# Optimization experiments

Measured on AMD Instinct MI355X. Metric: run time of the kernel, lower is better.

The kernel has to match this reference:

```python
import jax, jax.numpy as jnp
import numpy as np

HEADS = 4
DIM_HEAD = 32
GROUPS = 32  # min(256//4, 32)
EPS = 1e-5


def setup_inputs() -> dict:
    key = jax.random.key(0)
    ks = jax.random.split(key, 5)
    B, C, H, W = 16, 256, 64, 64
    CD, HC, WC = 512, 32, 32
    hid = HEADS * DIM_HEAD  # 128
    return {
        "x": jax.random.normal(ks[0], (B, C, H, W), jnp.float32),
        "cond": jax.random.normal(ks[1], (B, CD, HC, WC), jnp.float32),
        "gn_w": jnp.ones((C,), jnp.float32),
        "gn_b": jnp.zeros((C,), jnp.float32),
        "w_q": jax.random.normal(ks[2], (hid, C), jnp.float32) * 0.05,
        "b_q": jnp.zeros((hid,), jnp.float32),
        "w_kv": jax.random.normal(ks[3], (2 * hid, CD), jnp.float32) * 0.05,
        "b_kv": jnp.zeros((2 * hid,), jnp.float32),
        "w_out": jax.random.normal(ks[4], (C, hid), jnp.float32) * 0.05,
        "b_out": jnp.zeros((C,), jnp.float32),
    }


def _group_norm(x, w, b):
    # x: (B, C, H, W); normalize per group over (channels-in-group, H, W)
    B, C, H, W = x.shape
    xg = x.reshape(B, GROUPS, C // GROUPS, H, W)
    mu = jnp.mean(xg, axis=(2, 3, 4), keepdims=True)
    var = jnp.var(xg, axis=(2, 3, 4), keepdims=True)
    xn = ((xg - mu) * jax.lax.rsqrt(var + EPS)).reshape(B, C, H, W)
    return xn * w[None, :, None, None] + b[None, :, None, None]


def _conv1x1(x, w, b):
    # x: (B, Cin, H, W), w: (Cout, Cin), b: (Cout,)
    return jnp.einsum('oc,bchw->bohw', w, x) + b[None, :, None, None]


def reference(x, cond, gn_w, gn_b, w_q, b_q, w_kv, b_kv, w_out, b_out):
    B, C, H, W = x.shape
    hid = HEADS * DIM_HEAD
    xn = _group_norm(x, gn_w, gn_b)
    q = _conv1x1(xn, w_q, b_q)          # (B, hid, H, W)
    kv = _conv1x1(cond, w_kv, b_kv)     # (B, 2*hid, Hc, Wc)
    Nc = kv.shape[2] * kv.shape[3]
    N = H * W
    k = kv[:, :hid].reshape(B, HEADS, DIM_HEAD, Nc)
    v = kv[:, hid:].reshape(B, HEADS, DIM_HEAD, Nc)
    q = q.reshape(B, HEADS, DIM_HEAD, N)
    k = jax.nn.softmax(k, axis=-1)
    # kv outer product: (B, heads, d, e)
    context = jnp.einsum('bhdn,bhen->bhde', k, v)
    # query contraction over d: (B, heads, e, n)
    out = jnp.einsum('bhde,bhdn->bhen', context, q)
    out = out.reshape(B, hid, H, W)
    return _conv1x1(out, w_out, b_out)
```

## Files before the change

kernel.cpp:

```cpp
#include <hip/hip_runtime.h>
#include <hip/hip_bf16.h>

typedef __attribute__((ext_vector_type(8))) short bf16x8;
typedef __attribute__((ext_vector_type(4))) float f32x4;

__device__ __forceinline__ ushort f2bf(float f) {
    __hip_bfloat16 h = __float2bfloat16(f);
    return __builtin_bit_cast(ushort, h);
}
__device__ __forceinline__ float bflo(unsigned u) { return __uint_as_float(u << 16); }
__device__ __forceinline__ float bfhi(unsigned u) { return __uint_as_float(u & 0xffff0000u); }

__device__ __forceinline__ void unpack8(uint4 r, float* o) {
    o[0] = bflo(r.x); o[1] = bfhi(r.x); o[2] = bflo(r.y); o[3] = bfhi(r.y);
    o[4] = bflo(r.z); o[5] = bfhi(r.z); o[6] = bflo(r.w); o[7] = bfhi(r.w);
}

__device__ __forceinline__ void gload16(const void* g, void* l) {
    __builtin_amdgcn_global_load_lds(
        (const __attribute__((address_space(1))) unsigned*)g,
        (__attribute__((address_space(3))) unsigned*)l,
        16, 0, 0);
}

__global__ void cvtw_kernel(const float* __restrict__ w, ushort* __restrict__ o,
                            float* __restrict__ zbase) {
    int i = blockIdx.x * 256 + threadIdx.x;
    if (i < 68608) zbase[i] = 0.f;
    o[i] = f2bf(w[i]);
}

__global__ __launch_bounds__(256) void kvstats_kernel(const ushort* __restrict__ wkv16,
                                                      const float* __restrict__ cond,
                                                      const float* __restrict__ b_kv,
                                                      ushort* __restrict__ kv16,
                                                      const float* __restrict__ x,
                                                      float* __restrict__ statacc) {
    __shared__ ushort lA[64 * 64];
    __shared__ ushort lB[64 * 64];
    __shared__ float scratch[64 * 64];
    __shared__ float ls[4], lss[4];
    int bid = blockIdx.x;
    int t = threadIdx.x;
    if (bid < 1024) {
        int nb = bid & 15, ob = (bid >> 4) & 3, b = bid >> 6;
        int col0 = nb * 64, row0 = ob * 64;
        int l = t & 63, wid = t >> 6;
        int wr = wid >> 1, wc = wid & 1;
        int lr = l & 15, lg = l >> 4;
        const ushort* Ab = wkv16 + (size_t)row0 * 512;
        const float* Bb = cond + (size_t)b * 512 * 1024 + col0;
        int sp = t & 31, sj = t >> 5;
        f32x4 acc[2][2] = {};
        for (int k0 = 0; k0 < 512; k0 += 64) {
            #pragma unroll
            for (int j = 0; j < 2; ++j) {
                int gi = j * 256 + t;
                int r = gi >> 3, g = (gi & 7) ^ (r & 7);
                gload16(Ab + (size_t)r * 512 + k0 + g * 8, (char*)lA + gi * 16);
            }
            #pragma unroll
            for (int j = 0; j < 4; ++j) {
                int s = j * 256 + t;
                int r = s >> 4, g = s & 15;
                float4 v = *(const float4*)&Bb[(size_t)(k0 + r) * 1024 + g * 4];
                int gs = g ^ ((r >> 1) & 15);
                *(float4*)((char*)scratch + r * 256 + gs * 16) = v;
            }
            __syncthreads();
            {
                int swz = sp & 15;
                float4 a0 = *(const float4*)((char*)scratch + (2*sp) * 256 + ((2*sj) ^ swz) * 16);
                float4 a1 = *(const float4*)((char*)scratch + (2*sp) * 256 + ((2*sj+1) ^ swz) * 16);
                float4 b0 = *(const float4*)((char*)scratch + (2*sp+1) * 256 + ((2*sj) ^ swz) * 16);
                float4 b1 = *(const float4*)((char*)scratch + (2*sp+1) * 256 + ((2*sj+1) ^ swz) * 16);
                float c0v[8] = {a0.x, a0.y, a0.z, a0.w, a1.x, a1.y, a1.z, a1.w};
                float c1v[8] = {b0.x, b0.y, b0.z, b0.w, b1.x, b1.y, b1.z, b1.w};
                #pragma unroll
                for (int w = 0; w < 8; ++w) {
                    int n = sj * 8 + w;
                    unsigned pk = (unsigned)f2bf(c0v[w]) | ((unsigned)f2bf(c1v[w]) << 16);
                    *(unsigned*)((char*)lB + n * 128 + (((sp >> 2) ^ (n & 7)) * 16) + (sp & 3) * 4) = pk;
                }
            }
            __syncthreads();
            #pragma unroll
            for (int ks = 0; ks < 2; ++ks) {
                bf16x8 av[2], bv[2];
                #pragma unroll
                for (int mi = 0; mi < 2; ++mi) {
                    int ar = wr * 32 + mi * 16 + lr;
                    int q = (ks * 4 + lg) ^ (ar & 7);
                    av[mi] = *(const bf16x8*)((const char*)lA + ar * 128 + q * 16);
                }
                #pragma unroll
                for (int ni = 0; ni < 2; ++ni) {
                    int br = wc * 32 + ni * 16 + lr;
                    int q = (ks * 4 + lg) ^ (br & 7);
                    bv[ni] = *(const bf16x8*)((const char*)lB + br * 128 + q * 16);
                }
                #pragma unroll
                for (int mi = 0; mi < 2; ++mi)
                    #pragma unroll
                    for (int ni = 0; ni < 2; ++ni)
                        acc[mi][ni] = __builtin_amdgcn_mfma_f32_16x16x32_bf16(
                            av[mi], bv[ni], acc[mi][ni], 0, 0, 0);
            }
            __syncthreads();
        }
        int orow = row0 + wr * 32, ocol = col0 + wc * 32 + lr;
        #pragma unroll
        for (int mi = 0; mi < 2; ++mi) {
            int rb = orow + mi * 16 + lg * 4;
            float4 b4 = *(const float4*)&b_kv[rb];
            float bvr[4] = {b4.x, b4.y, b4.z, b4.w};
            #pragma unroll
            for (int ni = 0; ni < 2; ++ni) {
                int cc = ocol + ni * 16;
                #pragma unroll
                for (int r = 0; r < 4; ++r)
                    kv16[((size_t)b * 256 + rb + r) * 1024 + cc] = f2bf(acc[mi][ni][r] + bvr[r]);
            }
        }
    } else {
        int bg = bid - 1024;
        const float4* xp = (const float4*)(x + (size_t)bg * 32768);
        float s = 0.f, ss = 0.f;
        for (int i = t; i < 8192; i += 256) {
            float4 v = xp[i];
            s  += v.x + v.y + v.z + v.w;
            ss += v.x*v.x + v.y*v.y + v.z*v.z + v.w*v.w;
        }
        #pragma unroll
        for (int off = 32; off > 0; off >>= 1) {
            s  += __shfl_down(s, off, 64);
            ss += __shfl_down(ss, off, 64);
        }
        int wave = t >> 6;
        if ((t & 63) == 0) { ls[wave] = s; lss[wave] = ss; }
        __syncthreads();
        if (t == 0) {
            statacc[bg * 2]     = ls[0] + ls[1] + ls[2] + ls[3];
            statacc[bg * 2 + 1] = lss[0] + lss[1] + lss[2] + lss[3];
        }
    }
}

__global__ __launch_bounds__(256) void ctx_partial_kernel(const ushort* __restrict__ kv,
                                                          float* __restrict__ rowsum,
                                                          float* __restrict__ ctx) {
    int bh = blockIdx.y, b = bh >> 2, h = bh & 3;
    int n0 = blockIdx.x * 128;
    __shared__ float pl[32][129], vl[32][129];
    int t = threadIdx.x;
    int r = t >> 3, cs = (t & 7) * 16;
    const ushort* kp = kv + ((size_t)b * 256 + h * 32 + r) * 1024 + n0 + cs;
    const ushort* vp = kv + ((size_t)b * 256 + 128 + h * 32 + r) * 1024 + n0 + cs;
    float kvals[16], vvals[16];
    unpack8(((const uint4*)kp)[0], kvals);
    unpack8(((const uint4*)kp)[1], kvals + 8);
    unpack8(((const uint4*)vp)[0], vvals);
    unpack8(((const uint4*)vp)[1], vvals + 8);
    float psum = 0.f;
    #pragma unroll
    for (int i = 0; i < 16; ++i) {
        float e = __expf(kvals[i]);
        pl[r][cs + i] = e;
        vl[r][cs + i] = vvals[i];
        psum += e;
    }
    psum += __shfl_xor(psum, 1, 64);
    psum += __shfl_xor(psum, 2, 64);
    psum += __shfl_xor(psum, 4, 64);
    if ((t & 7) == 0) atomicAdd(&rowsum[bh * 32 + r], psum);
    __syncthreads();
    int d0 = t >> 5, e0 = t & 31;
    float acc[4] = {0.f, 0.f, 0.f, 0.f};
    #pragma unroll 8
    for (int nn = 0; nn < 128; ++nn) {
        float vv = vl[e0][nn];
        #pragma unroll
        for (int i = 0; i < 4; ++i)
            acc[i] += pl[d0 + 8 * i][nn] * vv;
    }
    #pragma unroll
    for (int i = 0; i < 4; ++i)
        atomicAdd(&ctx[((size_t)bh * 32 + d0 + 8 * i) * 32 + e0], acc[i]);
}

__global__ __launch_bounds__(256) void a_kernel(const float* __restrict__ ctx,
                                                const float* __restrict__ rowsum,
                                                const float* __restrict__ w_out,
                                                const float* __restrict__ w_q,
                                                const float* __restrict__ b_q,
                                                const float* __restrict__ statacc,
                                                const float* __restrict__ gn_w,
                                                const float* __restrict__ gn_b,
                                                const float* __restrict__ b_out,
                                                ushort* __restrict__ A16,
                                                float* __restrict__ biasb) {
    __shared__ float ctxl[4][32][33];
    __shared__ float wol[16][128];
    __shared__ float ml[16][128];
    __shared__ float cbuf[256][17];
    __shared__ float pbuf[16][17];
    int b = blockIdx.x >> 4, ot = (blockIdx.x & 15) << 4;
    int t = threadIdx.x;
    #pragma unroll
    for (int j = 0; j < 16; ++j) {
        int e = t + 256 * j;
        float inv = 1.f / rowsum[b * 128 + (e >> 5)];
        ctxl[e >> 10][(e >> 5) & 31][e & 31] = ctx[(size_t)b * 4096 + e] * inv;
    }
    #pragma unroll
    for (int j = 0; j < 8; ++j) {
        int e = t + 256 * j;
        wol[e >> 7][e & 127] = w_out[(ot + (e >> 7)) * 128 + (e & 127)];
    }
    __syncthreads();
    #pragma unroll
    for (int j = 0; j < 8; ++j) {
        int e = t + 256 * j;
        int o = e >> 7, hd = e & 127, h = hd >> 5, d = hd & 31;
        float acc = 0.f;
        #pragma unroll
        for (int ee = 0; ee < 32; ++ee) acc += wol[o][h * 32 + ee] * ctxl[h][d][ee];
        ml[o][hd] = acc;
    }
    __syncthreads();
    int c = t, g = c >> 3;
    float a0 = statacc[(b * 32 + g) * 2], a1 = statacc[(b * 32 + g) * 2 + 1];
    float mu  = a0 * (1.f / 32768.f);
    float var = a1 * (1.f / 32768.f) - mu * mu;
    float sc = rsqrtf(var + 1e-5f) * gn_w[c];
    float tc = gn_b[c] - mu * sc;
    float wt[16];
    #pragma unroll
    for (int o = 0; o < 16; ++o) wt[o] = 0.f;
    for (int hd = 0; hd < 128; ++hd) {
        float wq = w_q[hd * 256 + c];
        #pragma unroll
        for (int o = 0; o < 16; ++o) wt[o] += ml[o][hd] * wq;
    }
    ushort* Abp = A16 + ((size_t)b * 256 + ot) * 256 + c;
    #pragma unroll
    for (int o = 0; o < 16; ++o) {
        Abp[(size_t)o * 256] = f2bf(wt[o] * sc);
        cbuf[c][o] = wt[o] * tc;
    }
    __syncthreads();
    {
        int o = t >> 4, seg = t & 15;
        float p = 0.f;
        #pragma unroll
        for (int i = 0; i < 16; ++i) p += cbuf[seg * 16 + i][o];
        pbuf[o][seg] = p;
    }
    __syncthreads();
    if (t < 16) {
        int o = t;
        float sum = 0.f;
        #pragma unroll
        for (int s2 = 0; s2 < 16; ++s2) sum += pbuf[o][s2];
        float md = 0.f;
        #pragma unroll 8
        for (int hd = 0; hd < 128; ++hd) md += ml[o][hd] * b_q[hd];
        biasb[(size_t)b * 256 + ot + o] = sum + md + b_out[ot + o];
    }
}

__global__ __launch_bounds__(512) void out_gemm_fused(const ushort* __restrict__ A16,
                                                      const float* __restrict__ x,
                                                      const float* __restrict__ biasb,
                                                      float* __restrict__ out) {
    __shared__ ushort lA[256 * 64];
    __shared__ ushort lB[128 * 64];
    __shared__ float scratch[64 * 128];
    int b = blockIdx.y;
    int n0 = blockIdx.x * 128;
    int t = threadIdx.x;
    int l = t & 63, wid = t >> 6;
    int wr = wid >> 1, wc = wid & 1;
    int lr = l & 15, lg = l >> 4;
    const ushort* Ab = A16 + (size_t)b * 65536;
    const float* xb = x + (size_t)b * 256 * 4096 + n0;
    int sp = t & 31, sj = t >> 5;
    f32x4 acc[4][4] = {};
    for (int k0 = 0; k0 < 256; k0 += 64) {
        #pragma unroll
        for (int j = 0; j < 4; ++j) {
            int gi = j * 512 + t;
            int r = gi >> 3, g = (gi & 7) ^ (r & 7);
            gload16(Ab + (size_t)r * 256 + k0 + g * 8, (char*)lA + gi * 16);
        }
        #pragma unroll
        for (int j = 0; j < 4; ++j) {
            int s = j * 512 + t;
            int r = s >> 5, g = s & 31;
            float4 v = *(const float4*)&xb[(size_t)(k0 + r) * 4096 + g * 4];
            int gs = g ^ ((r >> 1) & 31);
            *(float4*)((char*)scratch + r * 512 + gs * 16) = v;
        }
        __syncthreads();
        {
            int swz = sp & 31;
            float4 a0 = *(const float4*)((char*)scratch + (2*sp) * 512 + ((2*sj) ^ swz) * 16);
            float4 a1 = *(const float4*)((char*)scratch + (2*sp) * 512 + ((2*sj+1) ^ swz) * 16);
            float4 b0 = *(const float4*)((char*)scratch + (2*sp+1) * 512 + ((2*sj) ^ swz) * 16);
            float4 b1 = *(const float4*)((char*)scratch + (2*sp+1) * 512 + ((2*sj+1) ^ swz) * 16);
            float c0v[8] = {a0.x, a0.y, a0.z, a0.w, a1.x, a1.y, a1.z, a1.w};
            float c1v[8] = {b0.x, b0.y, b0.z, b0.w, b1.x, b1.y, b1.z, b1.w};
            #pragma unroll
            for (int w = 0; w < 8; ++w) {
                int n = sj * 8 + w;
                unsigned pk = (unsigned)f2bf(c0v[w]) | ((unsigned)f2bf(c1v[w]) << 16);
                *(unsigned*)((char*)lB + n * 128 + (((sp >> 2) ^ (n & 7)) * 16) + (sp & 3) * 4) = pk;
            }
        }
        __syncthreads();
        #pragma unroll
        for (int ks = 0; ks < 2; ++ks) {
            bf16x8 av[4], bv[4];
            #pragma unroll
            for (int mi = 0; mi < 4; ++mi) {
                int ar = wr * 64 + mi * 16 + lr;
                int q = (ks * 4 + lg) ^ (ar & 7);
                av[mi] = *(const bf16x8*)((const char*)lA + ar * 128 + q * 16);
            }
            #pragma unroll
            for (int ni = 0; ni < 4; ++ni) {
                int br = wc * 64 + ni * 16 + lr;
                int q = (ks * 4 + lg) ^ (br & 7);
                bv[ni] = *(const bf16x8*)((const char*)lB + br * 128 + q * 16);
            }
            #pragma unroll
            for (int mi = 0; mi < 4; ++mi)
                #pragma unroll
                for (int ni = 0; ni < 4; ++ni)
                    acc[mi][ni] = __builtin_amdgcn_mfma_f32_16x16x32_bf16(
                        av[mi], bv[ni], acc[mi][ni], 0, 0, 0);
        }
        __syncthreads();
    }
    const float* bp = biasb + (size_t)b * 256;
    int orow = wr * 64, ocol = n0 + wc * 64 + lr;
    #pragma unroll
    for (int mi = 0; mi < 4; ++mi) {
        int rb = orow + mi * 16 + lg * 4;
        float4 b4 = *(const float4*)&bp[rb];
        float bvr[4] = {b4.x, b4.y, b4.z, b4.w};
        #pragma unroll
        for (int ni = 0; ni < 4; ++ni) {
            int cc = ocol + ni * 16;
            #pragma unroll
            for (int r = 0; r < 4; ++r)
                out[((size_t)b * 256 + rb + r) * 4096 + cc] = acc[mi][ni][r] + bvr[r];
        }
    }
}

extern "C" void kernel_launch(void* const* d_in, const int* in_sizes, int n_in,
                              void* d_out, int out_size, void* d_ws, size_t ws_size,
                              hipStream_t stream) {
    const float* x     = (const float*)d_in[0];
    const float* cond  = (const float*)d_in[1];
    const float* gn_w  = (const float*)d_in[2];
    const float* gn_b  = (const float*)d_in[3];
    const float* w_q   = (const float*)d_in[4];
    const float* b_q   = (const float*)d_in[5];
    const float* w_kv  = (const float*)d_in[6];
    const float* b_kv  = (const float*)d_in[7];
    const float* w_out = (const float*)d_in[8];
    const float* b_out = (const float*)d_in[9];
    float* out = (float*)d_out;

    float* f       = (float*)d_ws;
    float* statacc = f;
    float* rowsum  = f + 1024;
    float* ctx     = f + 3072;
    float* biasb   = f + 68608;
    ushort* u      = (ushort*)(f + 72704);
    ushort* wkv16  = u;
    ushort* kv16   = u + 131072;
    ushort* A16    = u + 4325376;

    cvtw_kernel<<<512, 256, 0, stream>>>(w_kv, wkv16, statacc);
    kvstats_kernel<<<1536, 256, 0, stream>>>(wkv16, cond, b_kv, kv16, x, statacc);
    ctx_partial_kernel<<<dim3(8, 64), 256, 0, stream>>>(kv16, rowsum, ctx);
    a_kernel<<<256, 256, 0, stream>>>(ctx, rowsum, w_out, w_q, b_q, statacc,
                                      gn_w, gn_b, b_out, A16, biasb);
    out_gemm_fused<<<dim3(32, 16), 512, 0, stream>>>(A16, x, biasb, out);
}
```

Measured before the change: 93.49 us.

## Register-prefetch next K tile in both GEMMs and split stats blocks with atomics

Both GEMM loops (kv projection and output GEMM) stop using direct global-to-LDS loads and instead prefetch the next K tile into registers right after the barrier, so global loads overlap the MFMA work on the current tile. The groupnorm statistics pass is split into four blocks per group that accumulate partial sums with atomicAdd, raising parallelism from 512 to 2048 stats blocks. The trade-off is higher register pressure and possibly lower occupancy, plus atomic float accumulation order that is not deterministic.

```diff
diff --git a/kernel.cpp b/kernel.cpp
--- a/kernel.cpp
+++ b/kernel.cpp
@@ -14,13 +14,6 @@
 __device__ __forceinline__ void unpack8(uint4 r, float* o) {
     o[0] = bflo(r.x); o[1] = bfhi(r.x); o[2] = bflo(r.y); o[3] = bfhi(r.y);
     o[4] = bflo(r.z); o[5] = bfhi(r.z); o[6] = bflo(r.w); o[7] = bfhi(r.w);
-}
-
-__device__ __forceinline__ void gload16(const void* g, void* l) {
-    __builtin_amdgcn_global_load_lds(
-        (const __attribute__((address_space(1))) unsigned*)g,
-        (__attribute__((address_space(3))) unsigned*)l,
-        16, 0, 0);
 }
 
 __global__ void cvtw_kernel(const float* __restrict__ w, ushort* __restrict__ o,
@@ -39,7 +32,7 @@
     __shared__ ushort lA[64 * 64];
     __shared__ ushort lB[64 * 64];
     __shared__ float scratch[64 * 64];
-    __shared__ float ls[4], lss[4];
+    __shared__ float red[8];
     int bid = blockIdx.x;
     int t = threadIdx.x;
     if (bid < 1024) {
@@ -51,23 +44,35 @@
         const ushort* Ab = wkv16 + (size_t)row0 * 512;
         const float* Bb = cond + (size_t)b * 512 * 1024 + col0;
         int sp = t & 31, sj = t >> 5;
+        uint4 aR[2]; float4 bR[4];
+        auto LOADA = [&](int k0) {
+            #pragma unroll
+            for (int j = 0; j < 2; ++j) {
+                int gi = j * 256 + t, r = gi >> 3, g = (gi & 7) ^ (r & 7);
+                aR[j] = *(const uint4*)(Ab + (size_t)r * 512 + k0 + g * 8);
+            }
+        };
+        auto LOADB = [&](int k0) {
+            #pragma unroll
+            for (int j = 0; j < 4; ++j) {
+                int s = j * 256 + t, r = s >> 4, g = s & 15;
+                bR[j] = *(const float4*)&Bb[(size_t)(k0 + r) * 1024 + g * 4];
+            }
+        };
+        LOADA(0); LOADB(0);
         f32x4 acc[2][2] = {};
-        for (int k0 = 0; k0 < 512; k0 += 64) {
-            #pragma unroll
-            for (int j = 0; j < 2; ++j) {
-                int gi = j * 256 + t;
-                int r = gi >> 3, g = (gi & 7) ^ (r & 7);
-                gload16(Ab + (size_t)r * 512 + k0 + g * 8, (char*)lA + gi * 16);
-            }
+        for (int it = 0; it < 8; ++it) {
+            #pragma unroll
+            for (int j = 0; j < 2; ++j)
+                *(uint4*)((char*)lA + (size_t)(j * 256 + t) * 16) = aR[j];
             #pragma unroll
             for (int j = 0; j < 4; ++j) {
-                int s = j * 256 + t;
-                int r = s >> 4, g = s & 15;
-                float4 v = *(const float4*)&Bb[(size_t)(k0 + r) * 1024 + g * 4];
+                int s = j * 256 + t, r = s >> 4, g = s & 15;
                 int gs = g ^ ((r >> 1) & 15);
-                *(float4*)((char*)scratch + r * 256 + gs * 16) = v;
+                *(float4*)((char*)scratch + r * 256 + gs * 16) = bR[j];
             }
             __syncthreads();
+            if (it < 7) { LOADA(it * 64 + 64); LOADB(it * 64 + 64); }
             {
                 int swz = sp & 15;
                 float4 a0 = *(const float4*)((char*)scratch + (2*sp) * 256 + ((2*sj) ^ swz) * 16);
@@ -123,11 +128,13 @@
             }
         }
     } else {
-        int bg = bid - 1024;
-        const float4* xp = (const float4*)(x + (size_t)bg * 32768);
+        int sid = bid - 1024;
+        int bg = sid >> 2, q = sid & 3;
+        const float4* xp = (const float4*)(x + (size_t)bg * 32768 + q * 8192);
         float s = 0.f, ss = 0.f;
-        for (int i = t; i < 8192; i += 256) {
-            float4 v = xp[i];
+        #pragma unroll
+        for (int j = 0; j < 8; ++j) {
+            float4 v = xp[t + 256 * j];
             s  += v.x + v.y + v.z + v.w;
             ss += v.x*v.x + v.y*v.y + v.z*v.z + v.w*v.w;
         }
@@ -137,11 +144,13 @@
             ss += __shfl_down(ss, off, 64);
         }
         int wave = t >> 6;
-        if ((t & 63) == 0) { ls[wave] = s; lss[wave] = ss; }
+        if ((t & 63) == 0) { red[wave * 2] = s; red[wave * 2 + 1] = ss; }
         __syncthreads();
         if (t == 0) {
-            statacc[bg * 2]     = ls[0] + ls[1] + ls[2] + ls[3];
-            statacc[bg * 2 + 1] = lss[0] + lss[1] + lss[2] + lss[3];
+            float S  = red[0] + red[2] + red[4] + red[6];
+            float SS = red[1] + red[3] + red[5] + red[7];
+            atomicAdd(&statacc[bg * 2],     S);
+            atomicAdd(&statacc[bg * 2 + 1], SS);
         }
     }
 }
@@ -285,23 +294,35 @@
     const ushort* Ab = A16 + (size_t)b * 65536;
     const float* xb = x + (size_t)b * 256 * 4096 + n0;
     int sp = t & 31, sj = t >> 5;
+    uint4 aR[4]; float4 bR[4];
+    auto LOADA = [&](int k0) {
+        #pragma unroll
+        for (int j = 0; j < 4; ++j) {
+            int gi = j * 512 + t, r = gi >> 3, g = (gi & 7) ^ (r & 7);
+            aR[j] = *(const uint4*)(Ab + (size_t)r * 256 + k0 + g * 8);
+        }
+    };
+    auto LOADB = [&](int k0) {
+        #pragma unroll
+        for (int j = 0; j < 4; ++j) {
+            int s = j * 512 + t, r = s >> 5, g = s & 31;
+            bR[j] = *(const float4*)&xb[(size_t)(k0 + r) * 4096 + g * 4];
+        }
+    };
+    LOADA(0); LOADB(0);
     f32x4 acc[4][4] = {};
-    for (int k0 = 0; k0 < 256; k0 += 64) {
+    for (int it = 0; it < 4; ++it) {
+        #pragma unroll
+        for (int j = 0; j < 4; ++j)
+            *(uint4*)((char*)lA + (size_t)(j * 512 + t) * 16) = aR[j];
         #pragma unroll
         for (int j = 0; j < 4; ++j) {
-            int gi = j * 512 + t;
-            int r = gi >> 3, g = (gi & 7) ^ (r & 7);
-            gload16(Ab + (size_t)r * 256 + k0 + g * 8, (char*)lA + gi * 16);
-        }
-        #pragma unroll
-        for (int j = 0; j < 4; ++j) {
-            int s = j * 512 + t;
-            int r = s >> 5, g = s & 31;
-            float4 v = *(const float4*)&xb[(size_t)(k0 + r) * 4096 + g * 4];
+            int s = j * 512 + t, r = s >> 5, g = s & 31;
             int gs = g ^ ((r >> 1) & 31);
-            *(float4*)((char*)scratch + r * 512 + gs * 16) = v;
+            *(float4*)((char*)scratch + r * 512 + gs * 16) = bR[j];
         }
         __syncthreads();
+        if (it < 3) { LOADA(it * 64 + 64); LOADB(it * 64 + 64); }
         {
             int swz = sp & 31;
             float4 a0 = *(const float4*)((char*)scratch + (2*sp) * 512 + ((2*sj) ^ swz) * 16);
@@ -385,7 +406,7 @@
     ushort* A16    = u + 4325376;
 
     cvtw_kernel<<<512, 256, 0, stream>>>(w_kv, wkv16, statacc);
-    kvstats_kernel<<<1536, 256, 0, stream>>>(wkv16, cond, b_kv, kv16, x, statacc);
+    kvstats_kernel<<<3072, 256, 0, stream>>>(wkv16, cond, b_kv, kv16, x, statacc);
     ctx_partial_kernel<<<dim3(8, 64), 256, 0, stream>>>(kv16, rowsum, ctx);
     a_kernel<<<256, 256, 0, stream>>>(ctx, rowsum, w_out, w_q, b_q, statacc,
                                       gn_w, gn_b, b_out, A16, biasb);
```

Result: slower. 151.8 us (+62.3%).
